# Optimization experiments

Measured on AMD Instinct MI355X. Metric: run time of the kernel, lower is better.

## Reference

```python
import jax, jax.numpy as jnp
import numpy as np

N = 100_000          # nodes
E = 1_600_000        # edges (avg degree 16)
F_RAW = 124          # float feature columns (after id column removed)
ID_DIM = 4
NF = F_RAW + ID_DIM  # encoder input features = 128
EMB = 64             # embedding_size, heads=1
L = 4                # num_layers
VOCAB = 2048         # id embedding table size
GAT_SLOPE = 0.2      # GATv2 attention leaky slope (PyG default)
ACT_SLOPE = 0.01     # nn.LeakyReLU default
EPS = 1e-5           # GraphNorm eps


def setup_inputs() -> dict:
    key = jax.random.key(0)
    ks = jax.random.split(key, 12)
    x_feat = jax.random.normal(ks[0], (N, F_RAW), jnp.float32)
    node_ids = jax.random.randint(ks[1], (N,), 0, VOCAB)
    edge_index = jax.random.randint(ks[2], (2, E), 0, N)
    emb_table = jax.random.normal(ks[3], (VOCAB, ID_DIM), jnp.float32) * 0.1
    w_in = jax.random.normal(ks[4], (NF, EMB), jnp.float32) / np.sqrt(NF)
    b_in = jnp.zeros((EMB,), jnp.float32)
    lin_w = jax.random.normal(ks[5], (L, EMB, EMB), jnp.float32) / np.sqrt(EMB)
    lin_b = jnp.zeros((L, EMB), jnp.float32)
    att = jax.random.normal(ks[6], (L, EMB), jnp.float32) / np.sqrt(EMB)
    conv_b = jnp.zeros((L, EMB), jnp.float32)
    gn_w = jnp.ones((L, EMB), jnp.float32)
    gn_b = jnp.zeros((L, EMB), jnp.float32)
    gn_ms = jnp.ones((L, EMB), jnp.float32)  # GraphNorm mean_scale
    return {"x_feat": x_feat, "node_ids": node_ids, "edge_index": edge_index,
            "emb_table": emb_table, "w_in": w_in, "b_in": b_in,
            "lin_w": lin_w, "lin_b": lin_b, "att": att, "conv_b": conv_b,
            "gn_w": gn_w, "gn_b": gn_b, "gn_ms": gn_ms}


def reference(x_feat, node_ids, edge_index, emb_table, w_in, b_in,
              lin_w, lin_b, att, conv_b, gn_w, gn_b, gn_ms):
    # id_encode: embedding lookup + concat with float features
    x = jnp.concatenate([x_feat, emb_table[node_ids]], axis=1)  # [N, 128]
    # encoder input projection (BatchNorm skipped: remove_random=True)
    x = jax.nn.leaky_relu(x @ w_in + b_in, ACT_SLOPE)           # [N, 64]
    n = x.shape[0]
    loops = jnp.arange(n)
    src = jnp.concatenate([edge_index[0], loops])               # add self loops
    dst = jnp.concatenate([edge_index[1], loops])
    h = None
    xs = []
    for l in range(L):
        # GATv2Conv, heads=1, share_weights=True (one shared linear)
        g = x @ lin_w[l] + lin_b[l]                             # [N, 64]
        e = jax.nn.leaky_relu(g[src] + g[dst], GAT_SLOPE) @ att[l]  # [E+N]
        # segment softmax over incoming edges per target node
        m = jax.ops.segment_max(e, dst, num_segments=n)
        ee = jnp.exp(e - m[dst])
        s = jax.ops.segment_sum(ee, dst, num_segments=n)
        alpha = ee / s[dst]                                     # [E+N]
        xs.append(alpha)
        x = jax.ops.segment_sum(alpha[:, None] * g[src], dst, num_segments=n) + conv_b[l]
        # GraphNorm (single graph: batch=None)
        mean = jnp.mean(x, axis=0)
        out = x - mean * gn_ms[l]
        var = jnp.mean(out * out, axis=0)
        x = out / jnp.sqrt(var + EPS) * gn_w[l] + gn_b[l]
        x = jax.nn.leaky_relu(x, ACT_SLOPE)
        # dropout p=0.3 is identity at inference
        h = x * 0.5 if h is None else h + x * 0.5
    return x, h, jnp.stack(xs, axis=0)  # ([N,64], [N,64], [L, E+N])
```

## Files before the change

kernel.cpp:

```cpp
#include <hip/hip_runtime.h>
#include <hip/hip_bf16.h>
#include <cstdint>

typedef __hip_bfloat16 bf16;
#define DEVI __device__ __forceinline__

DEVI float b2f(bf16 v){ return __bfloat162float(v); }
DEVI bf16 f2b(float v){ return __float2bfloat16(v); }
DEVI float lrelu(float x, float s){ return x > 0.f ? x : x * s; }

DEVI float ldf(const void* p, size_t i, int f){
  return f ? b2f(((const bf16*)p)[i]) : ((const float*)p)[i];
}
DEVI void stf(void* p, size_t i, int f, float v){
  if(f) ((bf16*)p)[i] = f2b(v); else ((float*)p)[i] = v;
}

DEVI float wave_sum(float v){
#pragma unroll
  for(int o = 32; o > 0; o >>= 1) v += __shfl_xor(v, o, 64);
  return v;
}
DEVI float qsum(float v){
  v += __shfl_xor(v, 1, 64);
  v += __shfl_xor(v, 2, 64);
  v += __shfl_xor(v, 4, 64);
  v += __shfl_xor(v, 8, 64);
  return v;
}

__global__ void k_detect(const uint32_t* __restrict__ xf, int* flag){
  const int lane = threadIdx.x & 63;
  float cnt = 0.f;
  for(int i = lane; i < 256; i += 64){
    uint32_t e = (xf[i] >> 7) & 0xFF;
    if(e >= 100 && e <= 140) cnt += 1.f;
  }
  cnt = wave_sum(cnt);
  if(lane == 0 && blockIdx.x == 0) *flag = (cnt > 180.f) ? 1 : 0;
}

__global__ __launch_bounds__(256) void k_encoder(
    const void* __restrict__ xf, const int* __restrict__ ids,
    const void* __restrict__ emb, const void* __restrict__ win,
    const void* __restrict__ bin, float* __restrict__ x,
    const int* __restrict__ flagp, int N)
{
  __shared__ float W[128*64];
  __shared__ float B[64];
  __shared__ float XR[4][128];
  const int t = threadIdx.x;
  const int f = *flagp;
  for(int i = t; i < 128*64; i += 256) W[i] = ldf(win, i, f);
  if(t < 64) B[t] = ldf(bin, t, f);
  __syncthreads();
  const int w = t >> 6, lane = t & 63;
  for(int base = blockIdx.x*4; base < N; base += gridDim.x*4){
    const int node = base + w;
    if(node < N){
      for(int k = lane; k < 128; k += 64){
        float v;
        if(k < 124) v = ldf(xf, (size_t)node*124 + k, f);
        else        v = ldf(emb, (size_t)ids[node]*4 + (k-124), f);
        XR[w][k] = v;
      }
      float acc = B[lane];
#pragma unroll 8
      for(int k = 0; k < 128; k++) acc = fmaf(XR[w][k], W[k*64+lane], acc);
      x[(size_t)node*64 + lane] = lrelu(acc, 0.01f);
    }
  }
}

__global__ __launch_bounds__(256) void k_linear(
    const float* __restrict__ x, const void* __restrict__ lw,
    const void* __restrict__ lb, float* __restrict__ g,
    const float* __restrict__ stats, const void* __restrict__ gw,
    const void* __restrict__ gb, const void* __restrict__ gms,
    void* __restrict__ out, const float* __restrict__ acsr,
    const int* __restrict__ pos, size_t h_base, size_t alpha_base,
    const int* __restrict__ flagp, int layer, int N, int T, float invN)
{
  __shared__ float W[64*64];
  __shared__ float B[64];
  __shared__ float XR[4][64];
  const int t = threadIdx.x;
  const int f = *flagp;
  const size_t wofs = (size_t)layer*64*64, bofs = (size_t)layer*64;
  for(int i = t; i < 64*64; i += 256) W[i] = ldf(lw, wofs + i, f);
  if(t < 64) B[t] = ldf(lb, bofs + t, f);
  const int w = t >> 6, lane = t & 63;
  float c = 0.f, a = 1.f, bb = 0.f;
  if(layer > 0){
    const int pl = layer - 1;
    const float* __restrict__ st = stats + (size_t)pl*1024;
    const size_t pofs = (size_t)pl*64;
    float s1 = 0.f, s2 = 0.f;
#pragma unroll
    for(int k = 0; k < 8; k++){ s1 += st[k*128 + lane]; s2 += st[k*128 + 64 + lane]; }
    const float mean = s1*invN, ex2 = s2*invN;
    c = mean * ldf(gms, pofs + lane, f);
    const float var = ex2 - 2.f*c*mean + c*c;
    a = ldf(gw, pofs + lane, f) / sqrtf(var + 1e-5f);
    bb = ldf(gb, pofs + lane, f);
  }
  __syncthreads();
  float wreg[64];
#pragma unroll
  for(int k = 0; k < 64; k++) wreg[k] = W[k*64 + lane];
  const float blane = B[lane];
  for(int base = blockIdx.x*4; base < N; base += gridDim.x*4){
    const int node = base + w;
    if(node < N){
      const size_t idx = (size_t)node*64 + lane;
      float v = x[idx];
      if(layer > 0){
        v = lrelu((v - c)*a + bb, 0.01f);
        float hv = 0.5f*v + (layer == 1 ? 0.f : ldf(out, h_base + idx, f));
        stf(out, h_base + idx, f, hv);
      }
      XR[w][lane] = v;
      float acc = blane;
      const float4* xr4 = (const float4*)XR[w];
#pragma unroll
      for(int k4 = 0; k4 < 16; k4++){
        const float4 xv = xr4[k4];
        acc = fmaf(xv.x, wreg[4*k4+0], acc);
        acc = fmaf(xv.y, wreg[4*k4+1], acc);
        acc = fmaf(xv.z, wreg[4*k4+2], acc);
        acc = fmaf(xv.w, wreg[4*k4+3], acc);
      }
      g[idx] = acc;
    }
  }
  if(layer > 0){
    for(size_t j = (size_t)blockIdx.x*256 + threadIdx.x; j < (size_t)T;
        j += (size_t)gridDim.x*256)
      stf(out, alpha_base + j, f, acsr[pos[j]]);
  }
}

__global__ void k_deg_init(int* deg, float* stats, int N){
  int i = blockIdx.x*blockDim.x + threadIdx.x;
  if(i < N) deg[i] = 1;
  if(i < 4096) stats[i] = 0.f;
}
__global__ void k_deg_count(const int* __restrict__ dst, int* deg, int E){
  int j = blockIdx.x*blockDim.x + threadIdx.x;
  if(j < E) atomicAdd(&deg[dst[j]], 1);
}
__global__ __launch_bounds__(256) void k_scan_partial(const int* __restrict__ deg, int* partial, int N){
  __shared__ int red[256];
  const int c = blockIdx.x, base = c*1024, t = threadIdx.x;
  int s = 0;
  for(int i = t; i < 1024; i += 256){ int idx = base+i; s += (idx < N) ? deg[idx] : 0; }
  red[t] = s; __syncthreads();
  for(int o = 128; o > 0; o >>= 1){ if(t < o) red[t] += red[t+o]; __syncthreads(); }
  if(t == 0) partial[c] = red[0];
}
__global__ __launch_bounds__(256) void k_scan_final(
    const int* __restrict__ deg, const int* __restrict__ partial,
    int* __restrict__ off, int* __restrict__ cur, int N, int nchunks)
{
  __shared__ int vals[1024];
  __shared__ int tsum[256];
  __shared__ int red[256];
  const int c = blockIdx.x, base = c*1024, t = threadIdx.x;
  red[t] = (t < c && t < nchunks) ? partial[t] : 0;
  for(int i = t; i < 1024; i += 256){ int idx = base+i; vals[i] = (idx < N) ? deg[idx] : 0; }
  __syncthreads();
  for(int o = 128; o > 0; o >>= 1){ if(t < o) red[t] += red[t+o]; __syncthreads(); }
  const int cbase = red[0];
  int a0 = vals[t*4], a1 = vals[t*4+1], a2 = vals[t*4+2], a3 = vals[t*4+3];
  int s = a0+a1+a2+a3;
  tsum[t] = s; __syncthreads();
  for(int o = 1; o < 256; o <<= 1){
    int v = (t >= o) ? tsum[t-o] : 0;
    __syncthreads();
    tsum[t] += v;
    __syncthreads();
  }
  int excl = tsum[t] - s + cbase;
  int o0 = excl, o1 = o0+a0, o2 = o1+a1, o3 = o2+a2;
  int idx = base + t*4;
  if(idx   < N){ off[idx]   = o0; cur[idx]   = o0; }
  if(idx+1 < N){ off[idx+1] = o1; cur[idx+1] = o1; }
  if(idx+2 < N){ off[idx+2] = o2; cur[idx+2] = o2; }
  if(idx+3 < N){ off[idx+3] = o3; cur[idx+3] = o3; }
}
__global__ void k_scatter(const int* __restrict__ src, const int* __restrict__ dst,
                          int* cur, int* __restrict__ pos, int* __restrict__ csrc,
                          int E, int N){
  int j = blockIdx.x*blockDim.x + threadIdx.x;
  int T = E + N;
  if(j >= T) return;
  int s, d;
  if(j < E){ s = src[j]; d = dst[j]; } else { s = j - E; d = s; }
  int p = atomicAdd(&cur[d], 1);
  csrc[p] = s;
  pos[j]  = p;
}

__global__ __launch_bounds__(256) void k_gat(
    const float* __restrict__ g, const int* __restrict__ off,
    const int* __restrict__ deg, const int* __restrict__ csrc,
    const void* __restrict__ att, const void* __restrict__ convb,
    float* __restrict__ xout, float* __restrict__ acsr,
    float* __restrict__ stats, const int* __restrict__ flagp,
    int layer, int N)
{
  __shared__ float sv[4][64], sv2[4][64];
  const int t = threadIdx.x, w = t >> 6, lane = t & 63;
  const int q = lane >> 4, L = lane & 15;
  const int f = *flagp;
  const size_t pofs = (size_t)layer*64;
  float* __restrict__ st = stats + (size_t)layer*1024;
  const int node = blockIdx.x*4 + w;
  const bool act = node < N;
  const int nc = act ? node : (N-1);

  float4 attv, cbv;
  attv.x = ldf(att, pofs + 4*L+0, f); attv.y = ldf(att, pofs + 4*L+1, f);
  attv.z = ldf(att, pofs + 4*L+2, f); attv.w = ldf(att, pofs + 4*L+3, f);
  cbv.x = ldf(convb, pofs + 4*L+0, f); cbv.y = ldf(convb, pofs + 4*L+1, f);
  cbv.z = ldf(convb, pofs + 4*L+2, f); cbv.w = ldf(convb, pofs + 4*L+3, f);

  const float4 gd = *(const float4*)(g + (size_t)nc*64 + 4*L);
  const int o = off[nc];
  const int d = act ? deg[nc] : 0;
  const int sreg = csrc[o + (lane < d ? lane : 0)];

  const int nitm = min((d + 7) >> 3, 8);

  float m0 = -1e30f, sp0 = 0.f, m1 = -1e30f, sp1 = 0.f, ereg = -1e30f;
  float4 ac0 = {0.f,0.f,0.f,0.f}, ac1 = {0.f,0.f,0.f,0.f};

  float4 rA0, rA1, rB0 = {0.f,0.f,0.f,0.f}, rB1 = {0.f,0.f,0.f,0.f};
  {
    const int s00 = __shfl(sreg, 2*q,   64);
    const int s01 = __shfl(sreg, 2*q+1, 64);
    rA0 = *(const float4*)(g + (size_t)s00*64 + 4*L);
    rA1 = *(const float4*)(g + (size_t)s01*64 + 4*L);
  }
  if(nitm > 1){
    const int s10 = __shfl(sreg, 8+2*q,   64);
    const int s11 = __shfl(sreg, 8+2*q+1, 64);
    rB0 = *(const float4*)(g + (size_t)s10*64 + 4*L);
    rB1 = *(const float4*)(g + (size_t)s11*64 + 4*L);
  }
  for(int i = 0; i < nitm; i++){
    float4 n0 = {0.f,0.f,0.f,0.f}, n1 = {0.f,0.f,0.f,0.f};
    const bool more = (i + 2) < nitm;
    if(more){
      const int t0 = __shfl(sreg, 8*(i+2)+2*q,   64);
      const int t1 = __shfl(sreg, 8*(i+2)+2*q+1, 64);
      n0 = *(const float4*)(g + (size_t)t0*64 + 4*L);
      n1 = *(const float4*)(g + (size_t)t1*64 + 4*L);
    }
    const int j0 = 8*i + 2*q;
    float pe0 = lrelu(rA0.x+gd.x, 0.2f)*attv.x + lrelu(rA0.y+gd.y, 0.2f)*attv.y
              + lrelu(rA0.z+gd.z, 0.2f)*attv.z + lrelu(rA0.w+gd.w, 0.2f)*attv.w;
    float pe1 = lrelu(rA1.x+gd.x, 0.2f)*attv.x + lrelu(rA1.y+gd.y, 0.2f)*attv.y
              + lrelu(rA1.z+gd.z, 0.2f)*attv.z + lrelu(rA1.w+gd.w, 0.2f)*attv.w;
    float e0 = qsum(pe0);
    float e1 = qsum(pe1);
    if(j0   >= d) e0 = -1e30f;
    if(j0+1 >= d) e1 = -1e30f;
    ereg = (L == 2*i  ) ? e0 : ereg;
    ereg = (L == 2*i+1) ? e1 : ereg;
    { const float mn = fmaxf(m0, e0);
      const float sc = __expf(m0 - mn), wt = __expf(e0 - mn);
      sp0   = sp0*sc   + wt;
      ac0.x = ac0.x*sc + wt*rA0.x; ac0.y = ac0.y*sc + wt*rA0.y;
      ac0.z = ac0.z*sc + wt*rA0.z; ac0.w = ac0.w*sc + wt*rA0.w;
      m0 = mn; }
    { const float mn = fmaxf(m1, e1);
      const float sc = __expf(m1 - mn), wt = __expf(e1 - mn);
      sp1   = sp1*sc   + wt;
      ac1.x = ac1.x*sc + wt*rA1.x; ac1.y = ac1.y*sc + wt*rA1.y;
      ac1.z = ac1.z*sc + wt*rA1.z; ac1.w = ac1.w*sc + wt*rA1.w;
      m1 = mn; }
    rA0 = rB0; rA1 = rB1;
    if(more){ rB0 = n0; rB1 = n1; }
  }
  float m = fmaxf(m0, m1), sp;
  float4 acc;
  {
    const float sA = __expf(m0 - m), sB = __expf(m1 - m);
    sp    = sp0*sA   + sp1*sB;
    acc.x = ac0.x*sA + ac1.x*sB; acc.y = ac0.y*sA + ac1.y*sB;
    acc.z = ac0.z*sA + ac1.z*sB; acc.w = ac0.w*sA + ac1.w*sB;
  }
#pragma unroll
  for(int ofs = 16; ofs <= 32; ofs <<= 1){
    const float m2  = __shfl_xor(m,  ofs, 64);
    const float sp2 = __shfl_xor(sp, ofs, 64);
    float4 a2;
    a2.x = __shfl_xor(acc.x, ofs, 64); a2.y = __shfl_xor(acc.y, ofs, 64);
    a2.z = __shfl_xor(acc.z, ofs, 64); a2.w = __shfl_xor(acc.w, ofs, 64);
    const float mn = fmaxf(m, m2);
    const float sA = __expf(m - mn), sB = __expf(m2 - mn);
    sp    = sp*sA    + sp2*sB;
    acc.x = acc.x*sA + a2.x*sB;
    acc.y = acc.y*sA + a2.y*sB;
    acc.z = acc.z*sA + a2.z*sB;
    acc.w = acc.w*sA + a2.w*sB;
    m = mn;
  }
  const float inv = 1.f / sp;

  if(act){
    const int jc = 4*(L & ~1) + 2*q + (L & 1);
    if(jc < d && jc < 64)
      acsr[o + jc] = __expf(ereg - m) * inv;
    for(int j2 = 64 + q; j2 < d; j2 += 4){
      const int s = csrc[o + j2];
      const float4 gs2 = *(const float4*)(g + (size_t)s*64 + 4*L);
      float pe = lrelu(gs2.x+gd.x, 0.2f)*attv.x + lrelu(gs2.y+gd.y, 0.2f)*attv.y
               + lrelu(gs2.z+gd.z, 0.2f)*attv.z + lrelu(gs2.w+gd.w, 0.2f)*attv.w;
      float e = qsum(pe);
      if(L == 0)
        acsr[o + j2] = __expf(e - m) * inv;
    }
  }
  float4 v4 = {0.f, 0.f, 0.f, 0.f};
  if(act){
    v4.x = acc.x*inv + cbv.x; v4.y = acc.y*inv + cbv.y;
    v4.z = acc.z*inv + cbv.z; v4.w = acc.w*inv + cbv.w;
    if(q == 0) *(float4*)(xout + (size_t)node*64 + 4*L) = v4;
  }
  if(q == 0){
    sv [w][4*L+0] = v4.x;      sv [w][4*L+1] = v4.y;
    sv [w][4*L+2] = v4.z;      sv [w][4*L+3] = v4.w;
    sv2[w][4*L+0] = v4.x*v4.x; sv2[w][4*L+1] = v4.y*v4.y;
    sv2[w][4*L+2] = v4.z*v4.z; sv2[w][4*L+3] = v4.w*v4.w;
  }
  __syncthreads();
  if(w == 0){
    float a = sv[0][lane]+sv[1][lane]+sv[2][lane]+sv[3][lane];
    float b = sv2[0][lane]+sv2[1][lane]+sv2[2][lane]+sv2[3][lane];
    const int bank = (blockIdx.x & 7) * 128;
    atomicAdd(&st[bank + lane],      a);
    atomicAdd(&st[bank + 64 + lane], b);
  }
}

__global__ __launch_bounds__(256) void k_gn_final(
    const float* __restrict__ x, const float* __restrict__ stats,
    const void* __restrict__ gw, const void* __restrict__ gb,
    const void* __restrict__ gms, void* __restrict__ out,
    const float* __restrict__ acsr, const int* __restrict__ pos,
    size_t x_base, size_t h_base, size_t alpha_base,
    const int* __restrict__ flagp, int N, int T, float invN)
{
  const int f = *flagp;
  const int lane = threadIdx.x & 63;
  const float* __restrict__ st = stats + (size_t)3*1024;
  const size_t pofs = (size_t)3*64;
  float s1 = 0.f, s2 = 0.f;
#pragma unroll
  for(int c = 0; c < 8; c++){
    s1 += st[c*128 + lane];
    s2 += st[c*128 + 64 + lane];
  }
  const float mean = s1 * invN;
  const float ex2  = s2 * invN;
  const float c    = mean * ldf(gms, pofs + lane, f);
  const float var  = ex2 - 2.f*c*mean + c*c;
  const float a    = ldf(gw, pofs + lane, f) / sqrtf(var + 1e-5f);
  const float bb   = ldf(gb, pofs + lane, f);
  const size_t total = (size_t)N * 64;
  for(size_t idx = (size_t)blockIdx.x*256 + threadIdx.x; idx < total;
      idx += (size_t)gridDim.x*256){
    float v = (x[idx] - c) * a + bb;
    v = lrelu(v, 0.01f);
    float hv = 0.5f*v + ldf(out, h_base + idx, f);
    stf(out, h_base + idx, f, hv);
    stf(out, x_base + idx, f, v);
  }
  for(size_t j = (size_t)blockIdx.x*256 + threadIdx.x; j < (size_t)T;
      j += (size_t)gridDim.x*256){
    stf(out, alpha_base + j, f, acsr[pos[j]]);
  }
}

extern "C" void kernel_launch(void* const* d_in, const int* in_sizes, int n_in,
                              void* d_out, int out_size, void* d_ws, size_t ws_size,
                              hipStream_t stream) {
  const void* xf   = d_in[0];
  const int*  ids  = (const int*)d_in[1];
  const int*  eidx = (const int*)d_in[2];
  const void* emb  = d_in[3];
  const void* win  = d_in[4];
  const void* bin  = d_in[5];
  const void* lw   = d_in[6];
  const void* lb   = d_in[7];
  const void* att  = d_in[8];
  const void* cb   = d_in[9];
  const void* gw   = d_in[10];
  const void* gb   = d_in[11];
  const void* gms  = d_in[12];

  const int N = in_sizes[1];
  const int E = in_sizes[2] / 2;
  const int T = E + N;
  const int* srcp = eidx;
  const int* dstp = eidx + E;

  char* p = (char*)d_ws;
  float* x  = (float*)p; p += (size_t)N*64*4;
  float* g  = (float*)p; p += (size_t)N*64*4;
  int* deg  = (int*)p;   p += ((size_t)N*4 + 63) & ~63ull;
  int* off  = (int*)p;   p += ((size_t)N*4 + 63) & ~63ull;
  int* cur  = (int*)p;   p += ((size_t)N*4 + 63) & ~63ull;
  int* pos  = (int*)p;   p += ((size_t)T*4 + 63) & ~63ull;
  int* csrc = (int*)p;   p += ((size_t)T*4 + 63) & ~63ull;
  float* acsr = (float*)p; p += ((size_t)T*4 + 63) & ~63ull;
  int* partial = (int*)p; p += 4096;
  float* stats = (float*)p; p += 4*1024*4;
  int* flag = (int*)p;   p += 64;

  const size_t x_base = 0;
  const size_t h_base = (size_t)N*64;
  const size_t a_base = (size_t)2*N*64;
  const float invN = 1.0f/(float)N;

  k_detect<<<1, 64, 0, stream>>>((const uint32_t*)xf, flag);
  k_encoder<<<2048, 256, 0, stream>>>(xf, ids, emb, win, bin, x, flag, N);

  k_deg_init <<<(N+255)/256, 256, 0, stream>>>(deg, stats, N);
  k_deg_count<<<(E+255)/256, 256, 0, stream>>>(dstp, deg, E);
  const int nchunks = (N + 1023) / 1024;
  k_scan_partial<<<nchunks, 256, 0, stream>>>(deg, partial, N);
  k_scan_final  <<<nchunks, 256, 0, stream>>>(deg, partial, off, cur, N, nchunks);
  k_scatter     <<<(T+255)/256, 256, 0, stream>>>(srcp, dstp, cur, pos, csrc, E, N);

  for(int l = 0; l < 4; l++){
    k_linear<<<2048, 256, 0, stream>>>(x, lw, lb, g, stats, gw, gb, gms,
                                       d_out, acsr, pos, h_base,
                                       a_base + (size_t)(l-1)*T,
                                       flag, l, N, T, invN);
    k_gat<<<(N+3)/4, 256, 0, stream>>>(g, off, deg, csrc, att, cb, x,
                                       acsr, stats, flag, l, N);
  }
  k_gn_final<<<1024, 256, 0, stream>>>(x, stats, gw, gb, gms, d_out,
                                       acsr, pos, x_base, h_base,
                                       a_base + (size_t)3*T, flag, N, T, invN);
}
```

Baseline: 1.047 ms.

## Make GAT kernel grid-stride persistent and accumulate GraphNorm stats per-thread

The GAT aggregation kernel now runs a fixed grid of 2048 blocks that loop over node groups, instead of one block per four nodes. Each wave keeps running sums and sums of squares in registers and issues the stats atomics once at the end. This removes the shared-memory reduction, the __syncthreads and the per-block atomics from every node group, which cuts atomic traffic on the stats banks by a large factor. The CSR scatter also uses a nontemporal store for csrc. The risk is worse load balance or latency hiding from fewer resident blocks, and the extra live registers in the loop.

```diff
diff --git a/kernel.cpp b/kernel.cpp
--- a/kernel.cpp
+++ b/kernel.cpp
@@ -197,7 +197,7 @@
   int s, d;
   if(j < E){ s = src[j]; d = dst[j]; } else { s = j - E; d = s; }
   int p = atomicAdd(&cur[d], 1);
-  csrc[p] = s;
+  __builtin_nontemporal_store(s, &csrc[p]);
   pos[j]  = p;
 }
 
@@ -209,15 +209,11 @@
     float* __restrict__ stats, const int* __restrict__ flagp,
     int layer, int N)
 {
-  __shared__ float sv[4][64], sv2[4][64];
   const int t = threadIdx.x, w = t >> 6, lane = t & 63;
   const int q = lane >> 4, L = lane & 15;
   const int f = *flagp;
   const size_t pofs = (size_t)layer*64;
   float* __restrict__ st = stats + (size_t)layer*1024;
-  const int node = blockIdx.x*4 + w;
-  const bool act = node < N;
-  const int nc = act ? node : (N-1);
 
   float4 attv, cbv;
   attv.x = ldf(att, pofs + 4*L+0, f); attv.y = ldf(att, pofs + 4*L+1, f);
@@ -225,123 +221,134 @@
   cbv.x = ldf(convb, pofs + 4*L+0, f); cbv.y = ldf(convb, pofs + 4*L+1, f);
   cbv.z = ldf(convb, pofs + 4*L+2, f); cbv.w = ldf(convb, pofs + 4*L+3, f);
 
-  const float4 gd = *(const float4*)(g + (size_t)nc*64 + 4*L);
-  const int o = off[nc];
-  const int d = act ? deg[nc] : 0;
-  const int sreg = csrc[o + (lane < d ? lane : 0)];
-
-  const int nitm = min((d + 7) >> 3, 8);
-
-  float m0 = -1e30f, sp0 = 0.f, m1 = -1e30f, sp1 = 0.f, ereg = -1e30f;
-  float4 ac0 = {0.f,0.f,0.f,0.f}, ac1 = {0.f,0.f,0.f,0.f};
-
-  float4 rA0, rA1, rB0 = {0.f,0.f,0.f,0.f}, rB1 = {0.f,0.f,0.f,0.f};
-  {
-    const int s00 = __shfl(sreg, 2*q,   64);
-    const int s01 = __shfl(sreg, 2*q+1, 64);
-    rA0 = *(const float4*)(g + (size_t)s00*64 + 4*L);
-    rA1 = *(const float4*)(g + (size_t)s01*64 + 4*L);
-  }
-  if(nitm > 1){
-    const int s10 = __shfl(sreg, 8+2*q,   64);
-    const int s11 = __shfl(sreg, 8+2*q+1, 64);
-    rB0 = *(const float4*)(g + (size_t)s10*64 + 4*L);
-    rB1 = *(const float4*)(g + (size_t)s11*64 + 4*L);
-  }
-  for(int i = 0; i < nitm; i++){
-    float4 n0 = {0.f,0.f,0.f,0.f}, n1 = {0.f,0.f,0.f,0.f};
-    const bool more = (i + 2) < nitm;
-    if(more){
-      const int t0 = __shfl(sreg, 8*(i+2)+2*q,   64);
-      const int t1 = __shfl(sreg, 8*(i+2)+2*q+1, 64);
-      n0 = *(const float4*)(g + (size_t)t0*64 + 4*L);
-      n1 = *(const float4*)(g + (size_t)t1*64 + 4*L);
-    }
-    const int j0 = 8*i + 2*q;
-    float pe0 = lrelu(rA0.x+gd.x, 0.2f)*attv.x + lrelu(rA0.y+gd.y, 0.2f)*attv.y
-              + lrelu(rA0.z+gd.z, 0.2f)*attv.z + lrelu(rA0.w+gd.w, 0.2f)*attv.w;
-    float pe1 = lrelu(rA1.x+gd.x, 0.2f)*attv.x + lrelu(rA1.y+gd.y, 0.2f)*attv.y
-              + lrelu(rA1.z+gd.z, 0.2f)*attv.z + lrelu(rA1.w+gd.w, 0.2f)*attv.w;
-    float e0 = qsum(pe0);
-    float e1 = qsum(pe1);
-    if(j0   >= d) e0 = -1e30f;
-    if(j0+1 >= d) e1 = -1e30f;
-    ereg = (L == 2*i  ) ? e0 : ereg;
-    ereg = (L == 2*i+1) ? e1 : ereg;
-    { const float mn = fmaxf(m0, e0);
-      const float sc = __expf(m0 - mn), wt = __expf(e0 - mn);
-      sp0   = sp0*sc   + wt;
-      ac0.x = ac0.x*sc + wt*rA0.x; ac0.y = ac0.y*sc + wt*rA0.y;
-      ac0.z = ac0.z*sc + wt*rA0.z; ac0.w = ac0.w*sc + wt*rA0.w;
-      m0 = mn; }
-    { const float mn = fmaxf(m1, e1);
-      const float sc = __expf(m1 - mn), wt = __expf(e1 - mn);
-      sp1   = sp1*sc   + wt;
-      ac1.x = ac1.x*sc + wt*rA1.x; ac1.y = ac1.y*sc + wt*rA1.y;
-      ac1.z = ac1.z*sc + wt*rA1.z; ac1.w = ac1.w*sc + wt*rA1.w;
-      m1 = mn; }
-    rA0 = rB0; rA1 = rB1;
-    if(more){ rB0 = n0; rB1 = n1; }
-  }
-  float m = fmaxf(m0, m1), sp;
-  float4 acc;
-  {
-    const float sA = __expf(m0 - m), sB = __expf(m1 - m);
-    sp    = sp0*sA   + sp1*sB;
-    acc.x = ac0.x*sA + ac1.x*sB; acc.y = ac0.y*sA + ac1.y*sB;
-    acc.z = ac0.z*sA + ac1.z*sB; acc.w = ac0.w*sA + ac1.w*sB;
-  }
-#pragma unroll
-  for(int ofs = 16; ofs <= 32; ofs <<= 1){
-    const float m2  = __shfl_xor(m,  ofs, 64);
-    const float sp2 = __shfl_xor(sp, ofs, 64);
-    float4 a2;
-    a2.x = __shfl_xor(acc.x, ofs, 64); a2.y = __shfl_xor(acc.y, ofs, 64);
-    a2.z = __shfl_xor(acc.z, ofs, 64); a2.w = __shfl_xor(acc.w, ofs, 64);
-    const float mn = fmaxf(m, m2);
-    const float sA = __expf(m - mn), sB = __expf(m2 - mn);
-    sp    = sp*sA    + sp2*sB;
-    acc.x = acc.x*sA + a2.x*sB;
-    acc.y = acc.y*sA + a2.y*sB;
-    acc.z = acc.z*sA + a2.z*sB;
-    acc.w = acc.w*sA + a2.w*sB;
-    m = mn;
-  }
-  const float inv = 1.f / sp;
-
-  if(act){
-    const int jc = 4*(L & ~1) + 2*q + (L & 1);
-    if(jc < d && jc < 64)
-      acsr[o + jc] = __expf(ereg - m) * inv;
-    for(int j2 = 64 + q; j2 < d; j2 += 4){
-      const int s = csrc[o + j2];
-      const float4 gs2 = *(const float4*)(g + (size_t)s*64 + 4*L);
-      float pe = lrelu(gs2.x+gd.x, 0.2f)*attv.x + lrelu(gs2.y+gd.y, 0.2f)*attv.y
-               + lrelu(gs2.z+gd.z, 0.2f)*attv.z + lrelu(gs2.w+gd.w, 0.2f)*attv.w;
-      float e = qsum(pe);
-      if(L == 0)
-        acsr[o + j2] = __expf(e - m) * inv;
-    }
-  }
-  float4 v4 = {0.f, 0.f, 0.f, 0.f};
-  if(act){
-    v4.x = acc.x*inv + cbv.x; v4.y = acc.y*inv + cbv.y;
-    v4.z = acc.z*inv + cbv.z; v4.w = acc.w*inv + cbv.w;
-    if(q == 0) *(float4*)(xout + (size_t)node*64 + 4*L) = v4;
+  float s1a[4] = {0.f,0.f,0.f,0.f};
+  float s2a[4] = {0.f,0.f,0.f,0.f};
+
+  const int ngrp = (N + 3) >> 2;
+  for(int grp = blockIdx.x; grp < ngrp; grp += gridDim.x){
+    const int node = grp*4 + w;
+    const bool act = node < N;
+    const int nc = act ? node : (N-1);
+
+    const float4 gd = *(const float4*)(g + (size_t)nc*64 + 4*L);
+    const int o = off[nc];
+    const int d = act ? deg[nc] : 0;
+    const int sreg = csrc[o + (lane < d ? lane : 0)];
+
+    const int nitm = min((d + 7) >> 3, 8);
+
+    float m0 = -1e30f, sp0 = 0.f, m1 = -1e30f, sp1 = 0.f, ereg = -1e30f;
+    float4 ac0 = {0.f,0.f,0.f,0.f}, ac1 = {0.f,0.f,0.f,0.f};
+
+    float4 rA0 = {0.f,0.f,0.f,0.f}, rA1 = rA0, rB0 = rA0, rB1 = rA0;
+    {
+      const int s00 = __shfl(sreg, 2*q,   64);
+      const int s01 = __shfl(sreg, 2*q+1, 64);
+      rA0 = *(const float4*)(g + (size_t)s00*64 + 4*L);
+      rA1 = *(const float4*)(g + (size_t)s01*64 + 4*L);
+    }
+    if(nitm > 1){
+      const int s10 = __shfl(sreg, 8+2*q,   64);
+      const int s11 = __shfl(sreg, 8+2*q+1, 64);
+      rB0 = *(const float4*)(g + (size_t)s10*64 + 4*L);
+      rB1 = *(const float4*)(g + (size_t)s11*64 + 4*L);
+    }
+    for(int i = 0; i < nitm; i++){
+      float4 n0 = {0.f,0.f,0.f,0.f}, n1 = {0.f,0.f,0.f,0.f};
+      const bool more = (i + 2) < nitm;
+      if(more){
+        const int t0 = __shfl(sreg, 8*(i+2)+2*q,   64);
+        const int t1 = __shfl(sreg, 8*(i+2)+2*q+1, 64);
+        n0 = *(const float4*)(g + (size_t)t0*64 + 4*L);
+        n1 = *(const float4*)(g + (size_t)t1*64 + 4*L);
+      }
+      const int j0 = 8*i + 2*q;
+      float pe0 = lrelu(rA0.x+gd.x, 0.2f)*attv.x + lrelu(rA0.y+gd.y, 0.2f)*attv.y
+                + lrelu(rA0.z+gd.z, 0.2f)*attv.z + lrelu(rA0.w+gd.w, 0.2f)*attv.w;
+      float pe1 = lrelu(rA1.x+gd.x, 0.2f)*attv.x + lrelu(rA1.y+gd.y, 0.2f)*attv.y
+                + lrelu(rA1.z+gd.z, 0.2f)*attv.z + lrelu(rA1.w+gd.w, 0.2f)*attv.w;
+      float e0 = qsum(pe0);
+      float e1 = qsum(pe1);
+      if(j0   >= d) e0 = -1e30f;
+      if(j0+1 >= d) e1 = -1e30f;
+      ereg = (L == 2*i  ) ? e0 : ereg;
+      ereg = (L == 2*i+1) ? e1 : ereg;
+      { const float mn = fmaxf(m0, e0);
+        const float sc = __expf(m0 - mn), wt = __expf(e0 - mn);
+        sp0   = sp0*sc   + wt;
+        ac0.x = ac0.x*sc + wt*rA0.x; ac0.y = ac0.y*sc + wt*rA0.y;
+        ac0.z = ac0.z*sc + wt*rA0.z; ac0.w = ac0.w*sc + wt*rA0.w;
+        m0 = mn; }
+      { const float mn = fmaxf(m1, e1);
+        const float sc = __expf(m1 - mn), wt = __expf(e1 - mn);
+        sp1   = sp1*sc   + wt;
+        ac1.x = ac1.x*sc + wt*rA1.x; ac1.y = ac1.y*sc + wt*rA1.y;
+        ac1.z = ac1.z*sc + wt*rA1.z; ac1.w = ac1.w*sc + wt*rA1.w;
+        m1 = mn; }
+      rA0 = rB0; rA1 = rB1;
+      if(more){ rB0 = n0; rB1 = n1; }
+    }
+    float m = fmaxf(m0, m1), sp;
+    float4 acc;
+    {
+      const float sA = __expf(m0 - m), sB = __expf(m1 - m);
+      sp    = sp0*sA   + sp1*sB;
+      acc.x = ac0.x*sA + ac1.x*sB; acc.y = ac0.y*sA + ac1.y*sB;
+      acc.z = ac0.z*sA + ac1.z*sB; acc.w = ac0.w*sA + ac1.w*sB;
+    }
+#pragma unroll
+    for(int ofs = 16; ofs <= 32; ofs <<= 1){
+      const float m2  = __shfl_xor(m,  ofs, 64);
+      const float sp2 = __shfl_xor(sp, ofs, 64);
+      float4 a2;
+      a2.x = __shfl_xor(acc.x, ofs, 64); a2.y = __shfl_xor(acc.y, ofs, 64);
+      a2.z = __shfl_xor(acc.z, ofs, 64); a2.w = __shfl_xor(acc.w, ofs, 64);
+      const float mn = fmaxf(m, m2);
+      const float sA = __expf(m - mn), sB = __expf(m2 - mn);
+      sp    = sp*sA    + sp2*sB;
+      acc.x = acc.x*sA + a2.x*sB;
+      acc.y = acc.y*sA + a2.y*sB;
+      acc.z = acc.z*sA + a2.z*sB;
+      acc.w = acc.w*sA + a2.w*sB;
+      m = mn;
+    }
+    const float inv = 1.f / sp;
+
+    if(act){
+      const int jc = 4*(L & ~1) + 2*q + (L & 1);
+      if(jc < d && jc < 64)
+        acsr[o + jc] = __expf(ereg - m) * inv;
+      for(int j2 = 64 + q; j2 < d; j2 += 4){
+        const int s = csrc[o + j2];
+        const float4 gs2 = *(const float4*)(g + (size_t)s*64 + 4*L);
+        float pe = lrelu(gs2.x+gd.x, 0.2f)*attv.x + lrelu(gs2.y+gd.y, 0.2f)*attv.y
+                 + lrelu(gs2.z+gd.z, 0.2f)*attv.z + lrelu(gs2.w+gd.w, 0.2f)*attv.w;
+        float e = qsum(pe);
+        if(L == 0)
+          acsr[o + j2] = __expf(e - m) * inv;
+      }
+      if(q == 0){
+        float4 v4;
+        v4.x = acc.x*inv + cbv.x; v4.y = acc.y*inv + cbv.y;
+        v4.z = acc.z*inv + cbv.z; v4.w = acc.w*inv + cbv.w;
+        *(float4*)(xout + (size_t)node*64 + 4*L) = v4;
+        s1a[0] += v4.x;      s1a[1] += v4.y;
+        s1a[2] += v4.z;      s1a[3] += v4.w;
+        s2a[0] += v4.x*v4.x; s2a[1] += v4.y*v4.y;
+        s2a[2] += v4.z*v4.z; s2a[3] += v4.w*v4.w;
+      }
+    }
   }
   if(q == 0){
-    sv [w][4*L+0] = v4.x;      sv [w][4*L+1] = v4.y;
-    sv [w][4*L+2] = v4.z;      sv [w][4*L+3] = v4.w;
-    sv2[w][4*L+0] = v4.x*v4.x; sv2[w][4*L+1] = v4.y*v4.y;
-    sv2[w][4*L+2] = v4.z*v4.z; sv2[w][4*L+3] = v4.w*v4.w;
-  }
-  __syncthreads();
-  if(w == 0){
-    float a = sv[0][lane]+sv[1][lane]+sv[2][lane]+sv[3][lane];
-    float b = sv2[0][lane]+sv2[1][lane]+sv2[2][lane]+sv2[3][lane];
     const int bank = (blockIdx.x & 7) * 128;
-    atomicAdd(&st[bank + lane],      a);
-    atomicAdd(&st[bank + 64 + lane], b);
+    atomicAdd(&st[bank + 4*L+0],      s1a[0]);
+    atomicAdd(&st[bank + 4*L+1],      s1a[1]);
+    atomicAdd(&st[bank + 4*L+2],      s1a[2]);
+    atomicAdd(&st[bank + 4*L+3],      s1a[3]);
+    atomicAdd(&st[bank + 64 + 4*L+0], s2a[0]);
+    atomicAdd(&st[bank + 64 + 4*L+1], s2a[1]);
+    atomicAdd(&st[bank + 64 + 4*L+2], s2a[2]);
+    atomicAdd(&st[bank + 64 + 4*L+3], s2a[3]);
   }
 }
 
@@ -440,8 +447,8 @@
                                        d_out, acsr, pos, h_base,
                                        a_base + (size_t)(l-1)*T,
                                        flag, l, N, T, invN);
-    k_gat<<<(N+3)/4, 256, 0, stream>>>(g, off, deg, csrc, att, cb, x,
-                                       acsr, stats, flag, l, N);
+    k_gat<<<2048, 256, 0, stream>>>(g, off, deg, csrc, att, cb, x,
+                                    acsr, stats, flag, l, N);
   }
   k_gn_final<<<1024, 256, 0, stream>>>(x, stats, gw, gb, gms, d_out,
                                        acsr, pos, x_base, h_base,
```

After: 1.325 ms. 26.7% more time.
